# Kernel tuning notes

Measured on AMD Instinct MI355X. Metric: run time of the kernel, lower is better.

Reference implementation:

```python
import jax, jax.numpy as jnp
import numpy as np

N_EMBD = 768
N_HEADS = 12
HEAD_DIM = N_EMBD // N_HEADS
B, T = 2, 4096


def setup_inputs() -> dict:
    key = jax.random.key(0)
    k1, k2, k3 = jax.random.split(key, 3)
    x = jax.random.normal(k1, (B, T, N_EMBD), dtype=jnp.float32)
    # torch Linear(in, out) weight has shape (out, in); x @ W.T == x @ W_j with W_j = W.T
    w_qkv = jax.random.normal(k2, (N_EMBD, 3 * N_EMBD), dtype=jnp.float32) * (1.0 / np.sqrt(N_EMBD))
    w_proj = jax.random.normal(k3, (N_EMBD, N_EMBD), dtype=jnp.float32) * (1.0 / np.sqrt(N_EMBD))
    return {"x": x, "w_qkv": w_qkv, "w_proj": w_proj}


def reference(x, w_qkv, w_proj):
    Bx, Tx, C = x.shape
    qkv = x @ w_qkv                                  # [B,T,3C]
    q, k, v = jnp.split(qkv, 3, axis=2)
    def to_heads(t):
        return t.reshape(Bx, Tx, N_HEADS, HEAD_DIM).transpose(0, 2, 1, 3)  # [B,H,T,D]
    q, k, v = to_heads(q), to_heads(k), to_heads(v)
    scale = HEAD_DIM ** -0.5
    att = jnp.einsum('bhqd,bhkd->bhqk', q, k) * scale  # [B,H,T,T]
    causal = jnp.tril(jnp.ones((Tx, Tx), dtype=bool))
    att = jnp.where(causal[None, None], att, -jnp.inf)
    att = jax.nn.softmax(att, axis=-1)
    y = jnp.einsum('bhqk,bhkd->bhqd', att, v)          # [B,H,T,D]
    y = y.transpose(0, 2, 1, 3).reshape(Bx, Tx, C)
    return y @ w_proj
```

## Files before the change

### kernel.cpp

```cpp
#include <hip/hip_runtime.h>
#include <hip/hip_bf16.h>

#define Bn 2
#define Tn 4096
#define Cn 768
#define Hn 12
#define Dn 64
#define Mn (Bn * Tn)
#define PAD 72

typedef __attribute__((ext_vector_type(8))) short bf16x8;
typedef __attribute__((ext_vector_type(4))) short bf16x4;
typedef __attribute__((ext_vector_type(4))) float f32x4;

typedef const __attribute__((address_space(1))) unsigned int* gas_ptr;
typedef __attribute__((address_space(3))) unsigned int* las_ptr;

__device__ __forceinline__ float b2f(unsigned short u) {
    return __uint_as_float(((unsigned int)u) << 16);
}
__device__ __forceinline__ unsigned short f2b(float f) {
    unsigned int x = __float_as_uint(f);
    x += 0x7FFFu + ((x >> 16) & 1u);
    return (unsigned short)(x >> 16);
}
__device__ __forceinline__ unsigned int cvt_pk_bf16(float lo, float hi) {
    unsigned int r;
    asm("v_cvt_pk_bf16_f32 %0, %1, %2" : "=v"(r) : "v"(lo), "v"(hi));
    return r;
}

__device__ __forceinline__ void async_ld16(const unsigned short* g, unsigned short* l) {
    __builtin_amdgcn_global_load_lds((gas_ptr)(const void*)g, (las_ptr)(void*)l, 16, 0, 0);
}

__global__ __launch_bounds__(256) void prep1_k(
    const void* __restrict__ wqkv, unsigned short* __restrict__ wqkvT,
    const void* __restrict__ x, unsigned short* __restrict__ xb,
    int* __restrict__ flag)
{
    __shared__ unsigned short Ts[64][PAD];
    __shared__ int anyf;
    const int tid = threadIdx.x;
    if (tid == 0) anyf = 0;
    __syncthreads();
    {
        int4 v = reinterpret_cast<const int4*>(wqkv)[tid];
        const unsigned short* u = reinterpret_cast<const unsigned short*>(&v);
        int bad = 0;
#pragma unroll
        for (int j = 0; j < 8; ++j) {
            const unsigned int e = (u[j] >> 7) & 0xFFu;
            bad |= (e >= 0x88u) ? 1 : 0;
        }
        if (bad) atomicOr(&anyf, 1);
    }
    __syncthreads();
    const bool f32 = (anyf != 0);
    if (tid == 0 && blockIdx.x == 0) *flag = anyf;

    if (blockIdx.x < 432) {
        const int K = Cn, N = 3 * Cn;
        const int nB = (blockIdx.x % 36) * 64, kB = (blockIdx.x / 36) * 64;
#pragma unroll
        for (int it = 0; it < 2; ++it) {
            const int r = (tid >> 3) + it * 32;
            const int c = (tid & 7) * 8;
            float t[8];
            if (f32) {
                const float* p = (const float*)wqkv + (size_t)(kB + r) * N + nB + c;
                float4 a = *reinterpret_cast<const float4*>(p);
                float4 b = *reinterpret_cast<const float4*>(p + 4);
                t[0]=a.x;t[1]=a.y;t[2]=a.z;t[3]=a.w;t[4]=b.x;t[5]=b.y;t[6]=b.z;t[7]=b.w;
            } else {
                int4 v = *reinterpret_cast<const int4*>((const unsigned short*)wqkv + (size_t)(kB + r) * N + nB + c);
                const unsigned short* u = reinterpret_cast<const unsigned short*>(&v);
#pragma unroll
                for (int j = 0; j < 8; ++j) t[j] = b2f(u[j]);
            }
#pragma unroll
            for (int j = 0; j < 8; ++j) Ts[c + j][r] = f2b(t[j]);
        }
        __syncthreads();
#pragma unroll
        for (int it = 0; it < 2; ++it) {
            const int n = (tid >> 3) + it * 32;
            const int k = (tid & 7) * 8;
            *reinterpret_cast<int4*>(wqkvT + (size_t)(nB + n) * K + kB + k) =
                *reinterpret_cast<const int4*>(&Ts[n][k]);
        }
    } else {
        const size_t i = ((size_t)(blockIdx.x - 432) * 256 + tid) * 8;
        union { int4 v; unsigned short u[8]; } pk;
        if (f32) {
            const float* p = (const float*)x + i;
            float4 a = *reinterpret_cast<const float4*>(p);
            float4 b = *reinterpret_cast<const float4*>(p + 4);
            float t[8] = {a.x, a.y, a.z, a.w, b.x, b.y, b.z, b.w};
#pragma unroll
            for (int j = 0; j < 8; ++j) pk.u[j] = f2b(t[j]);
        } else {
            pk.v = *reinterpret_cast<const int4*>((const unsigned short*)x + i);
        }
        *reinterpret_cast<int4*>(xb + i) = pk.v;
    }
}

__global__ __launch_bounds__(256) void transpose_w_k(
    const void* __restrict__ in, unsigned short* __restrict__ out,
    int K, int N, const int* __restrict__ flag)
{
    __shared__ unsigned short Ts[64][PAD];
    const int tid = threadIdx.x;
    const int kB = blockIdx.y * 64, nB = blockIdx.x * 64;
    const bool f32 = (*flag != 0);
#pragma unroll
    for (int it = 0; it < 2; ++it) {
        const int r = (tid >> 3) + it * 32;
        const int c = (tid & 7) * 8;
        float t[8];
        if (f32) {
            const float* p = (const float*)in + (size_t)(kB + r) * N + nB + c;
            float4 a = *reinterpret_cast<const float4*>(p);
            float4 b = *reinterpret_cast<const float4*>(p + 4);
            t[0]=a.x;t[1]=a.y;t[2]=a.z;t[3]=a.w;t[4]=b.x;t[5]=b.y;t[6]=b.z;t[7]=b.w;
        } else {
            int4 v = *reinterpret_cast<const int4*>((const unsigned short*)in + (size_t)(kB + r) * N + nB + c);
            const unsigned short* u = reinterpret_cast<const unsigned short*>(&v);
#pragma unroll
            for (int j = 0; j < 8; ++j) t[j] = b2f(u[j]);
        }
#pragma unroll
        for (int j = 0; j < 8; ++j) Ts[c + j][r] = f2b(t[j]);
    }
    __syncthreads();
#pragma unroll
    for (int it = 0; it < 2; ++it) {
        const int n = (tid >> 3) + it * 32;
        const int k = (tid & 7) * 8;
        *reinterpret_cast<int4*>(out + (size_t)(nB + n) * K + kB + k) =
            *reinterpret_cast<const int4*>(&Ts[n][k]);
    }
}

__global__ __launch_bounds__(256) void transpose_v_k(
    const unsigned short* __restrict__ Vin, unsigned short* __restrict__ Vt)
{
    __shared__ unsigned short Ts[64][PAD];
    const int tid = threadIdx.x;
    const size_t base = (size_t)blockIdx.y * Tn * Dn;
    const int t0 = blockIdx.x * 64;
#pragma unroll
    for (int it = 0; it < 2; ++it) {
        const int r = (tid >> 3) + it * 32;
        const int c = (tid & 7) * 8;
        int4 vv = *reinterpret_cast<const int4*>(Vin + base + (size_t)(t0 + r) * Dn + c);
        const unsigned short* u = reinterpret_cast<const unsigned short*>(&vv);
#pragma unroll
        for (int j = 0; j < 8; ++j) Ts[c + j][r] = u[j];
    }
    __syncthreads();
#pragma unroll
    for (int it = 0; it < 2; ++it) {
        const int d = (tid >> 3) + it * 32;
        const int tc = (tid & 7) * 8;
        *reinterpret_cast<int4*>(Vt + base + (size_t)d * Tn + t0 + tc) =
            *reinterpret_cast<const int4*>(&Ts[d][tc]);
    }
}

template <int EPI>
__global__ __launch_bounds__(256) void gemm_lds(
    const unsigned short* __restrict__ A, const unsigned short* __restrict__ Bt,
    void* __restrict__ Out, unsigned short* __restrict__ Qo,
    unsigned short* __restrict__ Ko, unsigned short* __restrict__ Vo,
    int M, int N, int K, const int* __restrict__ flag)
{
    __shared__ unsigned short As[8192];
    __shared__ unsigned short Bs[8192];
    const int tid = threadIdx.x;
    const int w = tid >> 6, l = tid & 63;
    const int l15 = l & 15, l4 = l >> 4;
    const int rowBase = blockIdx.y * 128;
    const int colBase = blockIdx.x * 128;
    const int mq = (w & 1) * 64, nq = (w >> 1) * 64;
    const bool f32 = (*flag != 0);

    const int laneRow = l15, laneK = l4 * 8;

    f32x4 acc[4][4];
#pragma unroll
    for (int i = 0; i < 4; ++i)
#pragma unroll
        for (int j = 0; j < 4; ++j) acc[i][j] = (f32x4){0.f, 0.f, 0.f, 0.f};

    for (int k0 = 0; k0 < K; k0 += 64) {
        __syncthreads();
#pragma unroll
        for (int j = 0; j < 4; ++j) {
            const int c = w * 4 + j;
            const int mt_g = c >> 1, kh = c & 1;
            const size_t ga = (size_t)(rowBase + mt_g * 16 + laneRow) * K + k0 + kh * 32 + laneK;
            const size_t gb = (size_t)(colBase + mt_g * 16 + laneRow) * K + k0 + kh * 32 + laneK;
            async_ld16(A + ga, &As[c * 512]);
            async_ld16(Bt + gb, &Bs[c * 512]);
        }
        __syncthreads();

#pragma unroll
        for (int kh = 0; kh < 2; ++kh) {
            bf16x8 af[4], bf[4];
#pragma unroll
            for (int mt = 0; mt < 4; ++mt)
                af[mt] = *reinterpret_cast<const bf16x8*>(
                    &As[(((mq >> 4) + mt) * 2 + kh) * 512 + l * 8]);
#pragma unroll
            for (int nt = 0; nt < 4; ++nt)
                bf[nt] = *reinterpret_cast<const bf16x8*>(
                    &Bs[(((nq >> 4) + nt) * 2 + kh) * 512 + l * 8]);
#pragma unroll
            for (int mt = 0; mt < 4; ++mt)
#pragma unroll
                for (int nt = 0; nt < 4; ++nt)
                    acc[mt][nt] = __builtin_amdgcn_mfma_f32_16x16x32_bf16(af[mt], bf[nt], acc[mt][nt], 0, 0, 0);
        }
    }

#pragma unroll
    for (int mt = 0; mt < 4; ++mt)
#pragma unroll
        for (int i = 0; i < 4; ++i) {
            const int m = rowBase + mq + mt * 16 + l4 * 4 + i;
#pragma unroll
            for (int nt = 0; nt < 4; ++nt) {
                const int n0 = colBase + nq + nt * 16 + l15;
                if (EPI == 0) {
                    if (f32) ((float*)Out)[(size_t)m * N + n0] = acc[mt][nt][i];
                    else ((unsigned short*)Out)[(size_t)m * N + n0] = f2b(acc[mt][nt][i]);
                } else {
                    const int sec = n0 / 768;
                    const int cc = n0 - sec * 768;
                    const int h = cc >> 6, d = cc & 63;
                    const int b = m >> 12, t = m & 4095;
                    unsigned short* dst = (sec == 0) ? Qo : (sec == 1) ? Ko : Vo;
                    dst[(((size_t)(b * Hn + h) * Tn + t) * Dn) + d] = f2b(acc[mt][nt][i]);
                }
            }
        }
}

__global__ __launch_bounds__(256) void gemm_qkv_fb(
    const void* __restrict__ A, const unsigned short* __restrict__ Bt,
    unsigned short* __restrict__ Qo, unsigned short* __restrict__ Ko,
    unsigned short* __restrict__ Vo, int M, int N, int K,
    const int* __restrict__ flag)
{
    __shared__ unsigned short As[128 * PAD];
    __shared__ unsigned short Bs[128 * PAD];
    const int tid = threadIdx.x;
    const int w = tid >> 6, l = tid & 63;
    const int l15 = l & 15, l4 = l >> 4;
    const int rowBase = blockIdx.y * 128;
    const int colBase = blockIdx.x * 128;
    const int mq = (w & 1) * 64, nq = (w >> 1) * 64;
    const bool af32 = (*flag != 0);

    f32x4 acc[4][4];
#pragma unroll
    for (int i = 0; i < 4; ++i)
#pragma unroll
        for (int j = 0; j < 4; ++j) acc[i][j] = (f32x4){0.f, 0.f, 0.f, 0.f};

    for (int k0 = 0; k0 < K; k0 += 64) {
        __syncthreads();
#pragma unroll
        for (int it = 0; it < 4; ++it) {
            const int s = tid + it * 256;
            const int r = s >> 3, c = (s & 7) * 8;
            union { int4 v; unsigned short u[8]; } pk;
            if (af32) {
                const float* p = (const float*)A + (size_t)(rowBase + r) * K + k0 + c;
                float4 a = *reinterpret_cast<const float4*>(p);
                float4 b = *reinterpret_cast<const float4*>(p + 4);
                float t[8] = {a.x, a.y, a.z, a.w, b.x, b.y, b.z, b.w};
#pragma unroll
                for (int j = 0; j < 8; ++j) pk.u[j] = f2b(t[j]);
            } else {
                pk.v = *reinterpret_cast<const int4*>(
                    (const unsigned short*)A + (size_t)(rowBase + r) * K + k0 + c);
            }
            *reinterpret_cast<int4*>(&As[r * PAD + c]) = pk.v;
            *reinterpret_cast<int4*>(&Bs[r * PAD + c]) =
                *reinterpret_cast<const int4*>(Bt + (size_t)(colBase + r) * K + k0 + c);
        }
        __syncthreads();
#pragma unroll
        for (int kk = 0; kk < 64; kk += 32) {
            bf16x8 af[4], bf[4];
#pragma unroll
            for (int mt = 0; mt < 4; ++mt)
                af[mt] = *reinterpret_cast<const bf16x8*>(&As[(mq + mt * 16 + l15) * PAD + kk + l4 * 8]);
#pragma unroll
            for (int nt = 0; nt < 4; ++nt)
                bf[nt] = *reinterpret_cast<const bf16x8*>(&Bs[(nq + nt * 16 + l15) * PAD + kk + l4 * 8]);
#pragma unroll
            for (int mt = 0; mt < 4; ++mt)
#pragma unroll
                for (int nt = 0; nt < 4; ++nt)
                    acc[mt][nt] = __builtin_amdgcn_mfma_f32_16x16x32_bf16(af[mt], bf[nt], acc[mt][nt], 0, 0, 0);
        }
    }

#pragma unroll
    for (int mt = 0; mt < 4; ++mt)
#pragma unroll
        for (int i = 0; i < 4; ++i) {
            const int m = rowBase + mq + mt * 16 + l4 * 4 + i;
#pragma unroll
            for (int nt = 0; nt < 4; ++nt) {
                const int n0 = colBase + nq + nt * 16 + l15;
                const int sec = n0 / 768;
                const int cc = n0 - sec * 768;
                const int h = cc >> 6, d = cc & 63;
                const int b = m >> 12, t = m & 4095;
                unsigned short* dst = (sec == 0) ? Qo : (sec == 1) ? Ko : Vo;
                dst[(((size_t)(b * Hn + h) * Tn + t) * Dn) + d] = f2b(acc[mt][nt][i]);
            }
        }
}

__global__ __launch_bounds__(256, 4) void attn_mfma2(
    const unsigned short* __restrict__ Q, const unsigned short* __restrict__ K,
    const unsigned short* __restrict__ Vt, unsigned short* __restrict__ Y)
{
    __shared__ unsigned short Ks[2][8 * 512];
    __shared__ unsigned short Vs[2][8 * 512];

    const int tid = threadIdx.x;
    const int w = tid >> 6, l = tid & 63;
    const int l15 = l & 15, l4 = l >> 4;

    const int f = (int)blockIdx.y * 32 + (int)blockIdx.x;
    const int r8 = f & 7, j = f >> 3;
    const int bh = r8 * 3 + (j >> 5);
    const int xq = j & 31;

    const size_t base = (size_t)bh * Tn * Dn;
    const float sc = 0.125f * 1.44269504088896f;
    const int b = bh / Hn, h = bh - b * Hn;

    const int vlb = (l4 >> 1) * 256 + l15 * 16 + (l4 & 1) * 8;

    for (int half = 0; half < 2; ++half) {
        const int t = half ? xq : (63 - xq);
        const int q0 = t * 64;
        const int qrow = q0 + w * 16 + l15;

        bf16x8 aq[2];
#pragma unroll
        for (int kh = 0; kh < 2; ++kh)
            aq[kh] = *reinterpret_cast<const bf16x8*>(
                Q + base + (size_t)qrow * Dn + kh * 32 + l4 * 8);

        f32x4 o[4];
#pragma unroll
        for (int dt = 0; dt < 4; ++dt) o[dt] = (f32x4){0.f, 0.f, 0.f, 0.f};
        float lsum = 0.f;

        const int nst = (q0 >> 6) + 1;

        __syncthreads();
#pragma unroll
        for (int jj = 0; jj < 2; ++jj) {
            const int c = w * 2 + jj;
            const int sub = c >> 1, kh = c & 1;
            async_ld16(K + base + (size_t)(sub * 16 + l15) * Dn + kh * 32 + l4 * 8,
                       &Ks[0][c * 512]);
            async_ld16(Vt + base + (size_t)(sub * 16 + l15) * Tn + kh * 32 + l4 * 8,
                       &Vs[0][c * 512]);
        }

        int cur = 0;
        for (int s = 0; s < nst; ++s) {
            const int k0 = s << 6;
            __syncthreads();

            if (s + 1 < nst) {
                const int kn = k0 + 64;
#pragma unroll
                for (int jj = 0; jj < 2; ++jj) {
                    const int c = w * 2 + jj;
                    const int sub = c >> 1, kh = c & 1;
                    async_ld16(K + base + (size_t)(kn + sub * 16 + l15) * Dn + kh * 32 + l4 * 8,
                               &Ks[cur ^ 1][c * 512]);
                    async_ld16(Vt + base + (size_t)(sub * 16 + l15) * Tn + kn + kh * 32 + l4 * 8,
                               &Vs[cur ^ 1][c * 512]);
                }
            }

            f32x4 sfr[4];
            __builtin_amdgcn_s_setprio(1);
#pragma unroll
            for (int tt = 0; tt < 4; ++tt) {
                bf16x8 ak0 = *reinterpret_cast<const bf16x8*>(&Ks[cur][(tt * 2 + 0) * 512 + l * 8]);
                bf16x8 ak1 = *reinterpret_cast<const bf16x8*>(&Ks[cur][(tt * 2 + 1) * 512 + l * 8]);
                f32x4 z = (f32x4){0.f, 0.f, 0.f, 0.f};
                z = __builtin_amdgcn_mfma_f32_16x16x32_bf16(ak0, aq[0], z, 0, 0, 0);
                z = __builtin_amdgcn_mfma_f32_16x16x32_bf16(ak1, aq[1], z, 0, 0, 0);
                sfr[tt] = z;
            }
            __builtin_amdgcn_s_setprio(0);

            const bool need_mask = (k0 + 63 > q0);
            float p[4][4];
#pragma unroll
            for (int tt = 0; tt < 4; ++tt)
#pragma unroll
                for (int i = 0; i < 4; ++i) {
                    float s2 = sfr[tt][i] * sc;
                    if (need_mask && (k0 + tt * 16 + l4 * 4 + i > qrow)) s2 = -1e30f;
                    const float e = __builtin_amdgcn_exp2f(s2);
                    p[tt][i] = e;
                    lsum += e;
                }

            bf16x4 pa[4];
#pragma unroll
            for (int tt = 0; tt < 4; ++tt) {
                union { unsigned int u[2]; bf16x4 v; } uu;
                uu.u[0] = cvt_pk_bf16(p[tt][0], p[tt][1]);
                uu.u[1] = cvt_pk_bf16(p[tt][2], p[tt][3]);
                pa[tt] = uu.v;
            }

            const char* vb = (const char*)&Vs[cur][0];
            __builtin_amdgcn_s_setprio(1);
#pragma unroll
            for (int dt = 0; dt < 4; ++dt) {
#pragma unroll
                for (int tt = 0; tt < 4; ++tt) {
                    bf16x4 bv = *reinterpret_cast<const bf16x4*>(vb + dt * 2048 + tt * 512 + vlb);
                    o[dt] = __builtin_amdgcn_mfma_f32_16x16x16bf16_1k(pa[tt], bv, o[dt], 0, 0, 0);
                }
            }
            __builtin_amdgcn_s_setprio(0);
            cur ^= 1;
        }

        lsum += __shfl_xor(lsum, 16);
        lsum += __shfl_xor(lsum, 32);

#pragma unroll
        for (int i = 0; i < 4; ++i) {
            const float lv = __shfl(lsum, (l & 48) + (l4 * 4 + i));
            const float inv = 1.0f / lv;
            const int row = q0 + w * 16 + l4 * 4 + i;
#pragma unroll
            for (int dt = 0; dt < 4; ++dt)
                Y[((size_t)(b * Tn + row)) * Cn + h * 64 + dt * 16 + l15] = f2b(o[dt][i] * inv);
        }
    }
}

__global__ __launch_bounds__(256, 3) void attn_mfma_fb(
    const unsigned short* __restrict__ Q, const unsigned short* __restrict__ K,
    const unsigned short* __restrict__ V, unsigned short* __restrict__ Y)
{
    __shared__ unsigned short Ks[96 * PAD];
    __shared__ unsigned short Vtl[96 * PAD];
    __shared__ unsigned short Ps[96 * PAD];

    const int tid = threadIdx.x;
    const int w = tid >> 6, l = tid & 63;
    const int l15 = l & 15, l4 = l >> 4;
    const int bh = blockIdx.y;
    const size_t base = (size_t)bh * Tn * Dn;
    const float sc = 0.125f * 1.44269504088896f;
    const int b = bh / Hn, h = bh - b * Hn;

    for (int half = 0; half < 2; ++half) {
        const int t = half ? (int)blockIdx.x : (63 - (int)blockIdx.x);
        const int q0 = t * 64;

        bf16x8 aq[2];
#pragma unroll
        for (int kh = 0; kh < 2; ++kh)
            aq[kh] = *reinterpret_cast<const bf16x8*>(
                Q + base + (size_t)(q0 + w * 16 + l15) * Dn + kh * 32 + l4 * 8);

        f32x4 o[4];
#pragma unroll
        for (int dt = 0; dt < 4; ++dt) o[dt] = (f32x4){0.f, 0.f, 0.f, 0.f};
        float l_i[4] = {0.f, 0.f, 0.f, 0.f};

        const int kend = q0 + 64;
        for (int k0 = 0; k0 < kend; k0 += 64) {
            __syncthreads();
#pragma unroll
            for (int it = 0; it < 2; ++it) {
                const int s = tid + it * 256;
                const int r = s >> 3, c = (s & 7) * 8;
                *reinterpret_cast<int4*>(&Ks[r * PAD + c]) =
                    *reinterpret_cast<const int4*>(K + base + (size_t)(k0 + r) * Dn + c);
            }
#pragma unroll
            for (int it = 0; it < 2; ++it) {
                const int r = tid & 63, d0 = (tid >> 6) * 8 + it * 32;
                int4 vv = *reinterpret_cast<const int4*>(V + base + (size_t)(k0 + r) * Dn + d0);
                const unsigned short* vu = reinterpret_cast<const unsigned short*>(&vv);
#pragma unroll
                for (int j = 0; j < 8; ++j) Vtl[(d0 + j) * PAD + r] = vu[j];
            }
            __syncthreads();

            f32x4 sfr[4];
#pragma unroll
            for (int tt = 0; tt < 4; ++tt) {
                bf16x8 bk0 = *reinterpret_cast<const bf16x8*>(&Ks[(tt * 16 + l15) * PAD + l4 * 8]);
                bf16x8 bk1 = *reinterpret_cast<const bf16x8*>(&Ks[(tt * 16 + l15) * PAD + 32 + l4 * 8]);
                f32x4 z = (f32x4){0.f, 0.f, 0.f, 0.f};
                z = __builtin_amdgcn_mfma_f32_16x16x32_bf16(aq[0], bk0, z, 0, 0, 0);
                z = __builtin_amdgcn_mfma_f32_16x16x32_bf16(aq[1], bk1, z, 0, 0, 0);
                sfr[tt] = z;
            }

            const bool need_mask = (k0 + 63 > q0);
            float p[4][4];
#pragma unroll
            for (int tt = 0; tt < 4; ++tt) {
                const int cb = k0 + tt * 16 + l15;
                const int rb = q0 + w * 16 + l4 * 4;
#pragma unroll
                for (int i = 0; i < 4; ++i) {
                    float s = sfr[tt][i] * sc;
                    if (need_mask && (cb > rb + i)) s = -1e30f;
                    const float e = exp2f(s);
                    p[tt][i] = e;
                    l_i[i] += e;
                }
            }

#pragma unroll
            for (int tt = 0; tt < 4; ++tt)
#pragma unroll
                for (int i = 0; i < 4; ++i)
                    Ps[(w * 16 + l4 * 4 + i) * PAD + tt * 16 + l15] = f2b(p[tt][i]);

            bf16x8 ap0 = *reinterpret_cast<const bf16x8*>(&Ps[(w * 16 + l15) * PAD + l4 * 8]);
            bf16x8 ap1 = *reinterpret_cast<const bf16x8*>(&Ps[(w * 16 + l15) * PAD + 32 + l4 * 8]);
#pragma unroll
            for (int dt = 0; dt < 4; ++dt) {
                bf16x8 bv0 = *reinterpret_cast<const bf16x8*>(&Vtl[(dt * 16 + l15) * PAD + l4 * 8]);
                bf16x8 bv1 = *reinterpret_cast<const bf16x8*>(&Vtl[(dt * 16 + l15) * PAD + 32 + l4 * 8]);
                o[dt] = __builtin_amdgcn_mfma_f32_16x16x32_bf16(ap0, bv0, o[dt], 0, 0, 0);
                o[dt] = __builtin_amdgcn_mfma_f32_16x16x32_bf16(ap1, bv1, o[dt], 0, 0, 0);
            }
        }

#pragma unroll
        for (int i = 0; i < 4; ++i)
#pragma unroll
            for (int off = 1; off < 16; off <<= 1) l_i[i] += __shfl_xor(l_i[i], off);

#pragma unroll
        for (int i = 0; i < 4; ++i) {
            const float inv = 1.0f / l_i[i];
            const int row = q0 + w * 16 + l4 * 4 + i;
#pragma unroll
            for (int dt = 0; dt < 4; ++dt)
                Y[((size_t)(b * Tn + row)) * Cn + h * 64 + dt * 16 + l15] = f2b(o[dt][i] * inv);
        }
    }
}

extern "C" void kernel_launch(void* const* d_in, const int* in_sizes, int n_in,
                              void* d_out, int out_size, void* d_ws, size_t ws_size,
                              hipStream_t stream)
{
    const void* x = d_in[0];
    const void* wqkv = d_in[1];
    const void* wproj = d_in[2];
    const size_t HSZ = (size_t)Bn * Hn * Tn * Dn;
    unsigned short* q = (unsigned short*)d_ws;
    unsigned short* k = q + HSZ;
    unsigned short* v = k + HSZ;
    unsigned short* R = v + HSZ;
    unsigned short* wqkvT = R;
    unsigned short* y = R;
    unsigned short* wprojT = q;
    const bool big = ws_size >= (size_t)5 * HSZ * 2 + 16;
    unsigned short* xb = R + HSZ;
    unsigned short* vt = xb;
    int* flag = big ? (int*)(xb + HSZ) : (int*)(R + HSZ);

    if (big) {
        prep1_k<<<3504, 256, 0, stream>>>(wqkv, wqkvT, x, xb, flag);
        gemm_lds<1><<<dim3(3 * Cn / 128, Mn / 128), 256, 0, stream>>>(
            xb, wqkvT, nullptr, q, k, v, Mn, 3 * Cn, Cn, flag);
        transpose_v_k<<<dim3(Tn / 64, Bn * Hn), 256, 0, stream>>>(v, vt);
        attn_mfma2<<<dim3(Tn / 128, Bn * Hn), 256, 0, stream>>>(q, k, vt, y);
    } else {
        prep1_k<<<432, 256, 0, stream>>>(wqkv, wqkvT, x, (unsigned short*)d_ws, flag);
        gemm_qkv_fb<<<dim3(3 * Cn / 128, Mn / 128), 256, 0, stream>>>(
            x, wqkvT, q, k, v, Mn, 3 * Cn, Cn, flag);
        attn_mfma_fb<<<dim3(Tn / 128, Bn * Hn), 256, 0, stream>>>(q, k, v, y);
    }
    transpose_w_k<<<dim3(Cn / 64, Cn / 64), 256, 0, stream>>>(wproj, wprojT, Cn, Cn, flag);
    gemm_lds<0><<<dim3(Cn / 128, Mn / 128), 256, 0, stream>>>(
        y, wprojT, d_out, nullptr, nullptr, nullptr, Mn, Cn, Cn, flag);
}
```

Measured before the change: 298.7 us.

## Fuse V transpose into QKV epilogue, merge wproj transpose into prep, remap workgroups

The QKV GEMM epilogue now writes V directly in transposed [B,H,D,T] layout with packed 8-byte stores, which removes the separate transpose_v_k launch and its round trip through memory. When the workspace is large enough, the w_proj transpose is folded into prep1_k as extra blocks, so transpose_w_k is no longer launched. The GEMM also remaps workgroup IDs in groups of 8, likely aimed at the MI355X XCD layout, to improve cache locality. The cost is an extra workspace region and transposed V stores that are less coalesced.

```diff
diff --git a/kernel.cpp b/kernel.cpp
--- a/kernel.cpp
+++ b/kernel.cpp
@@ -37,6 +37,7 @@
 __global__ __launch_bounds__(256) void prep1_k(
     const void* __restrict__ wqkv, unsigned short* __restrict__ wqkvT,
     const void* __restrict__ x, unsigned short* __restrict__ xb,
+    const void* __restrict__ wproj, unsigned short* __restrict__ wprojT,
     int* __restrict__ flag)
 {
     __shared__ unsigned short Ts[64][PAD];
@@ -59,37 +60,7 @@
     const bool f32 = (anyf != 0);
     if (tid == 0 && blockIdx.x == 0) *flag = anyf;
 
-    if (blockIdx.x < 432) {
-        const int K = Cn, N = 3 * Cn;
-        const int nB = (blockIdx.x % 36) * 64, kB = (blockIdx.x / 36) * 64;
-#pragma unroll
-        for (int it = 0; it < 2; ++it) {
-            const int r = (tid >> 3) + it * 32;
-            const int c = (tid & 7) * 8;
-            float t[8];
-            if (f32) {
-                const float* p = (const float*)wqkv + (size_t)(kB + r) * N + nB + c;
-                float4 a = *reinterpret_cast<const float4*>(p);
-                float4 b = *reinterpret_cast<const float4*>(p + 4);
-                t[0]=a.x;t[1]=a.y;t[2]=a.z;t[3]=a.w;t[4]=b.x;t[5]=b.y;t[6]=b.z;t[7]=b.w;
-            } else {
-                int4 v = *reinterpret_cast<const int4*>((const unsigned short*)wqkv + (size_t)(kB + r) * N + nB + c);
-                const unsigned short* u = reinterpret_cast<const unsigned short*>(&v);
-#pragma unroll
-                for (int j = 0; j < 8; ++j) t[j] = b2f(u[j]);
-            }
-#pragma unroll
-            for (int j = 0; j < 8; ++j) Ts[c + j][r] = f2b(t[j]);
-        }
-        __syncthreads();
-#pragma unroll
-        for (int it = 0; it < 2; ++it) {
-            const int n = (tid >> 3) + it * 32;
-            const int k = (tid & 7) * 8;
-            *reinterpret_cast<int4*>(wqkvT + (size_t)(nB + n) * K + kB + k) =
-                *reinterpret_cast<const int4*>(&Ts[n][k]);
-        }
-    } else {
+    if (blockIdx.x >= 432 && blockIdx.x < 3504) {
         const size_t i = ((size_t)(blockIdx.x - 432) * 256 + tid) * 8;
         union { int4 v; unsigned short u[8]; } pk;
         if (f32) {
@@ -103,17 +74,17 @@
             pk.v = *reinterpret_cast<const int4*>((const unsigned short*)x + i);
         }
         *reinterpret_cast<int4*>(xb + i) = pk.v;
-    }
-}
-
-__global__ __launch_bounds__(256) void transpose_w_k(
-    const void* __restrict__ in, unsigned short* __restrict__ out,
-    int K, int N, const int* __restrict__ flag)
-{
-    __shared__ unsigned short Ts[64][PAD];
-    const int tid = threadIdx.x;
-    const int kB = blockIdx.y * 64, nB = blockIdx.x * 64;
-    const bool f32 = (*flag != 0);
+        return;
+    }
+
+    const bool isW2 = (blockIdx.x >= 3504);
+    const void* in = isW2 ? wproj : wqkv;
+    unsigned short* out = isW2 ? wprojT : wqkvT;
+    const int K = Cn;
+    const int N = isW2 ? Cn : 3 * Cn;
+    const int id = isW2 ? ((int)blockIdx.x - 3504) : (int)blockIdx.x;
+    const int ncols = N / 64;
+    const int nB = (id % ncols) * 64, kB = (id / ncols) * 64;
 #pragma unroll
     for (int it = 0; it < 2; ++it) {
         const int r = (tid >> 3) + it * 32;
@@ -143,29 +114,40 @@
     }
 }
 
-__global__ __launch_bounds__(256) void transpose_v_k(
-    const unsigned short* __restrict__ Vin, unsigned short* __restrict__ Vt)
+__global__ __launch_bounds__(256) void transpose_w_k(
+    const void* __restrict__ in, unsigned short* __restrict__ out,
+    int K, int N, const int* __restrict__ flag)
 {
     __shared__ unsigned short Ts[64][PAD];
     const int tid = threadIdx.x;
-    const size_t base = (size_t)blockIdx.y * Tn * Dn;
-    const int t0 = blockIdx.x * 64;
+    const int kB = blockIdx.y * 64, nB = blockIdx.x * 64;
+    const bool f32 = (*flag != 0);
 #pragma unroll
     for (int it = 0; it < 2; ++it) {
         const int r = (tid >> 3) + it * 32;
         const int c = (tid & 7) * 8;
-        int4 vv = *reinterpret_cast<const int4*>(Vin + base + (size_t)(t0 + r) * Dn + c);
-        const unsigned short* u = reinterpret_cast<const unsigned short*>(&vv);
-#pragma unroll
-        for (int j = 0; j < 8; ++j) Ts[c + j][r] = u[j];
+        float t[8];
+        if (f32) {
+            const float* p = (const float*)in + (size_t)(kB + r) * N + nB + c;
+            float4 a = *reinterpret_cast<const float4*>(p);
+            float4 b = *reinterpret_cast<const float4*>(p + 4);
+            t[0]=a.x;t[1]=a.y;t[2]=a.z;t[3]=a.w;t[4]=b.x;t[5]=b.y;t[6]=b.z;t[7]=b.w;
+        } else {
+            int4 v = *reinterpret_cast<const int4*>((const unsigned short*)in + (size_t)(kB + r) * N + nB + c);
+            const unsigned short* u = reinterpret_cast<const unsigned short*>(&v);
+#pragma unroll
+            for (int j = 0; j < 8; ++j) t[j] = b2f(u[j]);
+        }
+#pragma unroll
+        for (int j = 0; j < 8; ++j) Ts[c + j][r] = f2b(t[j]);
     }
     __syncthreads();
 #pragma unroll
     for (int it = 0; it < 2; ++it) {
-        const int d = (tid >> 3) + it * 32;
-        const int tc = (tid & 7) * 8;
-        *reinterpret_cast<int4*>(Vt + base + (size_t)d * Tn + t0 + tc) =
-            *reinterpret_cast<const int4*>(&Ts[d][tc]);
+        const int n = (tid >> 3) + it * 32;
+        const int k = (tid & 7) * 8;
+        *reinterpret_cast<int4*>(out + (size_t)(nB + n) * K + kB + k) =
+            *reinterpret_cast<const int4*>(&Ts[n][k]);
     }
 }
 
@@ -181,8 +163,14 @@
     const int tid = threadIdx.x;
     const int w = tid >> 6, l = tid & 63;
     const int l15 = l & 15, l4 = l >> 4;
-    const int rowBase = blockIdx.y * 128;
-    const int colBase = blockIdx.x * 128;
+
+    const int gx = (int)gridDim.x;
+    const int nwg = gx * (int)gridDim.y;
+    int fid = (int)blockIdx.y * gx + (int)blockIdx.x;
+    if ((nwg & 7) == 0) fid = (fid & 7) * (nwg >> 3) + (fid >> 3);
+    const int rowBase = (fid / gx) * 128;
+    const int colBase = (fid % gx) * 128;
+
     const int mq = (w & 1) * 64, nq = (w >> 1) * 64;
     const bool f32 = (*flag != 0);
 
@@ -229,21 +217,33 @@
 #pragma unroll
     for (int mt = 0; mt < 4; ++mt)
 #pragma unroll
-        for (int i = 0; i < 4; ++i) {
-            const int m = rowBase + mq + mt * 16 + l4 * 4 + i;
-#pragma unroll
-            for (int nt = 0; nt < 4; ++nt) {
-                const int n0 = colBase + nq + nt * 16 + l15;
-                if (EPI == 0) {
-                    if (f32) ((float*)Out)[(size_t)m * N + n0] = acc[mt][nt][i];
-                    else ((unsigned short*)Out)[(size_t)m * N + n0] = f2b(acc[mt][nt][i]);
+        for (int nt = 0; nt < 4; ++nt) {
+            const int n0 = colBase + nq + nt * 16 + l15;
+            const int m0 = rowBase + mq + mt * 16 + l4 * 4;
+            if (EPI == 0) {
+#pragma unroll
+                for (int i = 0; i < 4; ++i) {
+                    if (f32) ((float*)Out)[(size_t)(m0 + i) * N + n0] = acc[mt][nt][i];
+                    else ((unsigned short*)Out)[(size_t)(m0 + i) * N + n0] = f2b(acc[mt][nt][i]);
+                }
+            } else {
+                const int sec = n0 / 768;
+                const int cc = n0 - sec * 768;
+                const int h = cc >> 6, d = cc & 63;
+                const int b = m0 >> 12, t0 = m0 & 4095;
+                if (sec < 2) {
+                    unsigned short* dst = (sec == 0) ? Qo : Ko;
+#pragma unroll
+                    for (int i = 0; i < 4; ++i)
+                        dst[(((size_t)(b * Hn + h) * Tn + t0 + i) * Dn) + d] = f2b(acc[mt][nt][i]);
                 } else {
-                    const int sec = n0 / 768;
-                    const int cc = n0 - sec * 768;
-                    const int h = cc >> 6, d = cc & 63;
-                    const int b = m >> 12, t = m & 4095;
-                    unsigned short* dst = (sec == 0) ? Qo : (sec == 1) ? Ko : Vo;
-                    dst[(((size_t)(b * Hn + h) * Tn + t) * Dn) + d] = f2b(acc[mt][nt][i]);
+                    union { unsigned int u[2]; uint2 v; } pk;
+                    pk.u[0] = (unsigned int)f2b(acc[mt][nt][0]) |
+                              ((unsigned int)f2b(acc[mt][nt][1]) << 16);
+                    pk.u[1] = (unsigned int)f2b(acc[mt][nt][2]) |
+                              ((unsigned int)f2b(acc[mt][nt][3]) << 16);
+                    *reinterpret_cast<uint2*>(
+                        &Vo[(((size_t)(b * Hn + h) * Dn + d) * Tn) + t0]) = pk.v;
                 }
             }
         }
@@ -590,22 +590,33 @@
     unsigned short* wprojT = q;
     const bool big = ws_size >= (size_t)5 * HSZ * 2 + 16;
     unsigned short* xb = R + HSZ;
-    unsigned short* vt = xb;
     int* flag = big ? (int*)(xb + HSZ) : (int*)(R + HSZ);
+    unsigned short* wprojT2 = xb + HSZ + 64;
+    const bool big2 = big &&
+        ws_size >= ((size_t)5 * HSZ + 64 + (size_t)Cn * Cn) * 2 + 16;
 
     if (big) {
-        prep1_k<<<3504, 256, 0, stream>>>(wqkv, wqkvT, x, xb, flag);
+        prep1_k<<<big2 ? 3648 : 3504, 256, 0, stream>>>(
+            wqkv, wqkvT, x, xb, wproj, big2 ? wprojT2 : xb, flag);
         gemm_lds<1><<<dim3(3 * Cn / 128, Mn / 128), 256, 0, stream>>>(
             xb, wqkvT, nullptr, q, k, v, Mn, 3 * Cn, Cn, flag);
-        transpose_v_k<<<dim3(Tn / 64, Bn * Hn), 256, 0, stream>>>(v, vt);
-        attn_mfma2<<<dim3(Tn / 128, Bn * Hn), 256, 0, stream>>>(q, k, vt, y);
+        attn_mfma2<<<dim3(Tn / 128, Bn * Hn), 256, 0, stream>>>(q, k, v, y);
+        if (big2) {
+            gemm_lds<0><<<dim3(Cn / 128, Mn / 128), 256, 0, stream>>>(
+                y, wprojT2, d_out, nullptr, nullptr, nullptr, Mn, Cn, Cn, flag);
+        } else {
+            transpose_w_k<<<dim3(Cn / 64, Cn / 64), 256, 0, stream>>>(wproj, wprojT, Cn, Cn, flag);
+            gemm_lds<0><<<dim3(Cn / 128, Mn / 128), 256, 0, stream>>>(
+                y, wprojT, d_out, nullptr, nullptr, nullptr, Mn, Cn, Cn, flag);
+        }
     } else {
-        prep1_k<<<432, 256, 0, stream>>>(wqkv, wqkvT, x, (unsigned short*)d_ws, flag);
+        prep1_k<<<432, 256, 0, stream>>>(wqkv, wqkvT, x, (unsigned short*)d_ws,
+                                         wproj, (unsigned short*)d_ws, flag);
         gemm_qkv_fb<<<dim3(3 * Cn / 128, Mn / 128), 256, 0, stream>>>(
             x, wqkvT, q, k, v, Mn, 3 * Cn, Cn, flag);
         attn_mfma_fb<<<dim3(Tn / 128, Bn * Hn), 256, 0, stream>>>(q, k, v, y);
-    }
-    transpose_w_k<<<dim3(Cn / 64, Cn / 64), 256, 0, stream>>>(wproj, wprojT, Cn, Cn, flag);
-    gemm_lds<0><<<dim3(Cn / 128, Mn / 128), 256, 0, stream>>>(
-        y, wprojT, d_out, nullptr, nullptr, nullptr, Mn, Cn, Cn, flag);
-}
+        transpose_w_k<<<dim3(Cn / 64, Cn / 64), 256, 0, stream>>>(wproj, wprojT, Cn, Cn, flag);
+        gemm_lds<0><<<dim3(Cn / 128, Mn / 128), 256, 0, stream>>>(
+            y, wprojT, d_out, nullptr, nullptr, nullptr, Mn, Cn, Cn, flag);
+    }
+}
```

Result: faster. 287.5 us (-3.8%).
